# Performance work log

Hardware: AMD Instinct MI355X
Metric: run time of the kernel (lower is better)

The kernel has to match this reference:

```python
import jax, jax.numpy as jnp
import numpy as np

H2 = 512    # internal hidden = hidden_size*2
E = 128     # embedding_size
V = 50000   # vocabulary_size
L = 512     # max_length (encoder input length)
B = 128     # batch


def setup_inputs() -> dict:
    key = jax.random.key(0)
    ks = jax.random.split(key, 20)
    s = 0.02
    return {
        "input_ids": jax.random.randint(ks[0], (B,), 0, V),
        "hidden": jax.random.normal(ks[1], (1, B, H2), jnp.float32),
        "encoder_outputs": jax.random.normal(ks[2], (L, B, H2), jnp.float32),
        "full_input": jax.random.randint(ks[3], (L, B), 0, V),
        # parameters
        "embedding": jax.random.normal(ks[4], (V, E), jnp.float32) * s,
        "W_ih": jax.random.normal(ks[5], (3 * H2, E), jnp.float32) * s,
        "W_hh": jax.random.normal(ks[6], (3 * H2, H2), jnp.float32) * s,
        "b_ih": jnp.zeros((3 * H2,), jnp.float32),
        "b_hh": jnp.zeros((3 * H2,), jnp.float32),
        "W_ds": jax.random.normal(ks[7], (H2, H2), jnp.float32) * s,
        "b_ds": jnp.zeros((H2,), jnp.float32),
        "w_h": jax.random.normal(ks[8], (H2,), jnp.float32),
        "att_v": jax.random.normal(ks[9], (H2,), jnp.float32),
        "W_oh": jax.random.normal(ks[10], (E, 2 * H2), jnp.float32) * s,
        "b_oh": jnp.zeros((E,), jnp.float32),
        "W_ov": jax.random.normal(ks[11], (V, E), jnp.float32) * s,
        "b_ov": jnp.zeros((V,), jnp.float32),
        "W_ptr": jax.random.normal(ks[12], (1, 2 * H2 + E), jnp.float32) * s,
        "b_ptr": jnp.zeros((1,), jnp.float32),
    }


def reference(input_ids, hidden, encoder_outputs, full_input, embedding,
              W_ih, W_hh, b_ih, b_hh, W_ds, b_ds, w_h, att_v,
              W_oh, b_oh, W_ov, b_ov, W_ptr, b_ptr):
    Bn = input_ids.shape[0]
    Ln = encoder_outputs.shape[0]
    Vn = embedding.shape[0]

    emb = embedding[input_ids]                       # [B, E] (dropout = identity in eval)
    h0 = hidden[0]                                   # [B, 2h]

    # single GRU step (PyTorch gate order r, z, n)
    gx = emb @ W_ih.T + b_ih                         # [B, 3*2h]
    gh = h0 @ W_hh.T + b_hh
    xr, xz, xn = jnp.split(gx, 3, axis=1)
    hr, hz, hn = jnp.split(gh, 3, axis=1)
    r = jax.nn.sigmoid(xr + hr)
    z = jax.nn.sigmoid(xz + hz)
    n = jnp.tanh(xn + r * hn)
    h_new = (1.0 - z) * n + z * h0                   # [B, 2h]

    # Bahdanau-style attention (faithful to source, incl. softmax over dim=1 = batch axis)
    dsl = h_new @ W_ds.T + b_ds                      # [B, 2h]
    att = jnp.tanh(w_h * encoder_outputs + dsl[None])  # [L, B, 2h]
    scores = (att_v * att).sum(-1)                   # [L, B]
    attn = jax.nn.softmax(scores, axis=1)            # torch F.softmax(dim=1)

    context = jnp.einsum('lb,lbh->bh', attn, encoder_outputs)  # [B, 2h]
    combined = jnp.concatenate([h_new, context], axis=1)        # [B, 4h]

    p_vocab = jax.nn.softmax((combined @ W_oh.T + b_oh) @ W_ov.T + b_ov, axis=1)  # [B, V]

    p_gen = jax.nn.sigmoid(jnp.concatenate([combined, emb], axis=1) @ W_ptr.T + b_ptr)  # [B, 1]

    # scatter attention mass onto extended vocab (copy distribution)
    token_input_dist = jnp.zeros((Bn, Vn + Ln), p_vocab.dtype).at[
        jnp.arange(Bn)[:, None], full_input.T
    ].add(attn.T)

    pad = jnp.zeros((Bn, Ln), p_vocab.dtype)
    p_final = jnp.concatenate([p_vocab * p_gen, pad], axis=1) + (1.0 - p_gen) * token_input_dist
    return (p_final, h_new[None], attn)
```

## Files before the change

### kernel.cpp

```cpp
#include <hip/hip_runtime.h>
#include <math.h>

#define B_  128
#define E_  128
#define H2_ 512
#define H3_ 1536
#define L_  512
#define V_  50000
#define VL_ 50512

typedef short bf16x8 __attribute__((ext_vector_type(8)));
typedef float f32x4 __attribute__((ext_vector_type(4)));

__device__ __forceinline__ float fast_tanh(float x) {
    float e = __expf(2.f * x);
    return 1.f - 2.f / (e + 1.f);
}
__device__ __forceinline__ float fast_sigmoid(float x) {
    return 1.f / (1.f + __expf(-x));
}
__device__ __forceinline__ short f2bf(float f) {
    unsigned u = __float_as_uint(f);
    u += 0x7fff + ((u >> 16) & 1);
    return (short)(u >> 16);
}

__global__ void k_init(float* __restrict__ gx, float* __restrict__ gh,
                       float* __restrict__ dsl, float* __restrict__ hid,
                       float* __restrict__ out, float* __restrict__ rsum8,
                       const float* __restrict__ b_ih, const float* __restrict__ b_hh,
                       const float* __restrict__ b_ds, const float* __restrict__ b_oh) {
    int i = blockIdx.x * blockDim.x + threadIdx.x;
    if (i < 196608) { gx[i] = b_ih[i % 1536]; return; }
    i -= 196608;
    if (i < 196608) { gh[i] = b_hh[i % 1536]; return; }
    i -= 196608;
    if (i < 65536)  { dsl[i] = b_ds[i & 511]; return; }
    i -= 65536;
    if (i < 16384)  { hid[i] = b_oh[i & 127]; return; }
    i -= 16384;
    if (i < 65536)  { out[(size_t)(i >> 9) * VL_ + V_ + (i & 511)] = 0.f; return; }
    i -= 65536;
    if (i < 1024)   rsum8[i] = 0.f;
}

__global__ void k_gates(const int* __restrict__ ids, const float* __restrict__ tab,
                        const float* __restrict__ hidden,
                        const float* __restrict__ W_ih, const float* __restrict__ W_hh,
                        float* __restrict__ gx, float* __restrict__ gh) {
    __shared__ float As[32][36];
    __shared__ float Ws[32][36];
    int z = blockIdx.z;
    int which = (z < 2) ? 0 : 1;
    int kbeg  = which ? (z - 2) * 128 : z * 64;
    int kiter = which ? 4 : 2;
    const float* W = which ? W_hh : W_ih;
    int ldw = which ? H2_ : E_;
    float* C = which ? gh : gx;
    int bm = blockIdx.x * 32, bn = blockIdx.y * 32;
    int tid = threadIdx.x;
    int tm0 = (tid / 16) * 2, tn0 = (tid % 16) * 2;
    float acc[2][2] = {};
    for (int it = 0; it < kiter; ++it) {
        int k0 = kbeg + it * 32;
        for (int v = tid; v < 256; v += 256) {
            int m = v >> 3, q = (v & 7) << 2;
            int gm = bm + m;
            const float* arow = which ? (hidden + (size_t)gm * H2_)
                                      : (tab + (size_t)ids[gm] * E_);
            float4 x = *(const float4*)(arow + k0 + q);
            As[q+0][m] = x.x; As[q+1][m] = x.y; As[q+2][m] = x.z; As[q+3][m] = x.w;
        }
        for (int v = tid; v < 256; v += 256) {
            int n = v >> 3, q = (v & 7) << 2;
            float4 x = *(const float4*)(W + (size_t)(bn + n) * ldw + k0 + q);
            Ws[q+0][n] = x.x; Ws[q+1][n] = x.y; Ws[q+2][n] = x.z; Ws[q+3][n] = x.w;
        }
        __syncthreads();
        #pragma unroll
        for (int kk = 0; kk < 32; ++kk) {
            float a0 = As[kk][tm0], a1 = As[kk][tm0+1];
            float w0 = Ws[kk][tn0], w1 = Ws[kk][tn0+1];
            acc[0][0] += a0*w0; acc[0][1] += a0*w1;
            acc[1][0] += a1*w0; acc[1][1] += a1*w1;
        }
        __syncthreads();
    }
    #pragma unroll
    for (int i = 0; i < 2; ++i)
        #pragma unroll
        for (int j = 0; j < 2; ++j)
            atomicAdd(&C[(size_t)(bm+tm0+i) * H3_ + bn+tn0+j], acc[i][j]);
}

template<int BM, int BN, int BK, int TM, int TN, int SPLITK>
__global__ void gemm_t(const float* __restrict__ A, int lda,
                       const float* __restrict__ W, int ldw,
                       float* __restrict__ C, int ldc,
                       int N, int K) {
    __shared__ float As[BK][BM + 4];
    __shared__ float Ws[BK][BN + 4];
    int bm = blockIdx.x * BM, bn = blockIdx.y * BN;
    int tid = threadIdx.x;
    constexpr int NT = BN / TN;
    int tm0 = (tid / NT) * TM;
    int tn0 = (tid % NT) * TN;
    int kchunk = K / SPLITK;
    int kbeg = blockIdx.z * kchunk;
    float acc[TM][TN] = {};
    for (int k0 = kbeg; k0 < kbeg + kchunk; k0 += BK) {
        #pragma unroll
        for (int v = tid; v < BM * BK / 4; v += 256) {
            int m = v / (BK / 4), q = (v % (BK / 4)) * 4;
            float4 x = *(const float4*)(A + (size_t)(bm + m) * lda + k0 + q);
            As[q+0][m] = x.x; As[q+1][m] = x.y; As[q+2][m] = x.z; As[q+3][m] = x.w;
        }
        #pragma unroll
        for (int v = tid; v < BN * BK / 4; v += 256) {
            int n = v / (BK / 4), q = (v % (BK / 4)) * 4;
            float4 x = *(const float4*)(W + (size_t)(bn + n) * ldw + k0 + q);
            Ws[q+0][n] = x.x; Ws[q+1][n] = x.y; Ws[q+2][n] = x.z; Ws[q+3][n] = x.w;
        }
        __syncthreads();
        #pragma unroll
        for (int kk = 0; kk < BK; ++kk) {
            float a[TM], w[TN];
            #pragma unroll
            for (int i = 0; i < TM; ++i) a[i] = As[kk][tm0 + i];
            #pragma unroll
            for (int j = 0; j < TN; ++j) w[j] = Ws[kk][tn0 + j];
            #pragma unroll
            for (int i = 0; i < TM; ++i)
                #pragma unroll
                for (int j = 0; j < TN; ++j) acc[i][j] += a[i] * w[j];
        }
        __syncthreads();
    }
    #pragma unroll
    for (int i = 0; i < TM; ++i)
        #pragma unroll
        for (int j = 0; j < TN; ++j)
            atomicAdd(&C[(size_t)(bm+tm0+i) * ldc + bn+tn0+j], acc[i][j]);
}

__global__ void k_gru(const float* __restrict__ gx, const float* __restrict__ gh,
                      const float* __restrict__ h0,
                      float* __restrict__ comb, float* __restrict__ hout) {
    int idx = blockIdx.x * blockDim.x + threadIdx.x;
    int b = idx >> 9, h = idx & 511;
    const float* gxb = gx + b * H3_;
    const float* ghb = gh + b * H3_;
    float xr = gxb[h], xz = gxb[H2_ + h], xn = gxb[2 * H2_ + h];
    float hr = ghb[h], hz = ghb[H2_ + h], hn = ghb[2 * H2_ + h];
    float r = fast_sigmoid(xr + hr);
    float z = fast_sigmoid(xz + hz);
    float n = fast_tanh(xn + r * hn);
    float hv = (1.f - z) * n + z * h0[idx];
    comb[b * (2 * H2_) + h] = hv;
    comb[b * (2 * H2_) + H2_ + h] = 0.f;
    hout[idx] = hv;
}

__global__ void k_scores(const float* __restrict__ enc, const float* __restrict__ dsl,
                         const float* __restrict__ w_h, const float* __restrict__ att_v,
                         float* __restrict__ scores) {
    int wid = (blockIdx.x << 2) + (threadIdx.x >> 6);
    int lane = threadIdx.x & 63;
    int l = wid >> 7, b = wid & 127;
    const float4* e4 = (const float4*)(enc + ((size_t)(l * B_ + b)) * H2_);
    const float4* d4 = (const float4*)(dsl + b * H2_);
    const float4* w4 = (const float4*)w_h;
    const float4* v4 = (const float4*)att_v;
    float s = 0.f;
    #pragma unroll
    for (int i = 0; i < 2; ++i) {
        int j = lane + (i << 6);
        float4 e = e4[j], d = d4[j], w = w4[j], v = v4[j];
        s += v.x * fast_tanh(w.x * e.x + d.x);
        s += v.y * fast_tanh(w.y * e.y + d.y);
        s += v.z * fast_tanh(w.z * e.z + d.z);
        s += v.w * fast_tanh(w.w * e.w + d.w);
    }
    #pragma unroll
    for (int o = 32; o; o >>= 1) s += __shfl_xor(s, o);
    if (lane == 0) scores[l * B_ + b] = s;
}

__global__ void k_softmax(const float* __restrict__ scores, float* __restrict__ attn) {
    int l = blockIdx.x, lane = threadIdx.x;
    float s0 = scores[l * B_ + lane], s1 = scores[l * B_ + lane + 64];
    float m = fmaxf(s0, s1);
    #pragma unroll
    for (int o = 32; o; o >>= 1) m = fmaxf(m, __shfl_xor(m, o));
    float e0 = __expf(s0 - m), e1 = __expf(s1 - m);
    float t = e0 + e1;
    #pragma unroll
    for (int o = 32; o; o >>= 1) t += __shfl_xor(t, o);
    float inv = 1.f / t;
    attn[l * B_ + lane] = e0 * inv;
    attn[l * B_ + lane + 64] = e1 * inv;
}

__global__ void k_context(const float* __restrict__ enc, const float* __restrict__ attn,
                          float* __restrict__ comb) {
    int b = blockIdx.x;
    int l0 = blockIdx.y << 6;
    int tid = threadIdx.x;
    __shared__ float a_s[64];
    if (tid < 64) a_s[tid] = attn[(l0 + tid) * B_ + b];
    __syncthreads();
    const float4* e = (const float4*)(enc + ((size_t)l0 * B_ + b) * H2_) + tid;
    float4 c = make_float4(0.f, 0.f, 0.f, 0.f);
    #pragma unroll 8
    for (int i = 0; i < 64; ++i) {
        float4 x = e[(size_t)i * (B_ * H2_ / 4)];
        float a = a_s[i];
        c.x += a * x.x; c.y += a * x.y; c.z += a * x.z; c.w += a * x.w;
    }
    float* dst = comb + b * (2 * H2_) + H2_ + tid * 4;
    atomicAdd(dst + 0, c.x); atomicAdd(dst + 1, c.y);
    atomicAdd(dst + 2, c.z); atomicAdd(dst + 3, c.w);
}

__global__ void k_pgen(const float* __restrict__ comb,
                       const int* __restrict__ ids, const float* __restrict__ tab,
                       const float* __restrict__ W_ptr, const float* __restrict__ b_ptr,
                       float* __restrict__ pgen) {
    int b = blockIdx.x, lane = threadIdx.x;
    float s = 0.f;
    for (int j = lane; j < 2 * H2_; j += 64) s += W_ptr[j] * comb[b * (2 * H2_) + j];
    const float* erow = tab + (size_t)ids[b] * E_;
    for (int j = lane; j < E_; j += 64) s += W_ptr[2 * H2_ + j] * erow[j];
    #pragma unroll
    for (int o = 32; o; o >>= 1) s += __shfl_xor(s, o);
    if (lane == 0) pgen[b] = fast_sigmoid(s + b_ptr[0]);
}

__global__ void k_vocab(const float* __restrict__ hid, const float* __restrict__ Wov,
                        const float* __restrict__ bov, float* __restrict__ out,
                        float* __restrict__ rsum8) {
    __shared__ float sm[4][128];
    int L = threadIdx.x & 63, w = threadIdx.x >> 6;
    int lrow = L & 15, lk = L >> 4;
    int n0 = blockIdx.x * 128 + w * 32;

    bf16x8 bfr[2][4];
    #pragma unroll
    for (int nt = 0; nt < 2; ++nt) {
        int n = n0 + nt * 16 + lrow;
        #pragma unroll
        for (int kk = 0; kk < 4; ++kk) {
            bf16x8 f;
            if (n < V_) {
                const float* p = Wov + (size_t)n * 128 + kk * 32 + lk * 8;
                float4 x = *(const float4*)p, y = *(const float4*)(p + 4);
                f[0]=f2bf(x.x); f[1]=f2bf(x.y); f[2]=f2bf(x.z); f[3]=f2bf(x.w);
                f[4]=f2bf(y.x); f[5]=f2bf(y.y); f[6]=f2bf(y.z); f[7]=f2bf(y.w);
            } else {
                #pragma unroll
                for (int j = 0; j < 8; ++j) f[j] = 0;
            }
            bfr[nt][kk] = f;
        }
    }
    f32x4 acc[8][2] = {};
    #pragma unroll
    for (int mt = 0; mt < 8; ++mt) {
        bf16x8 afr[4];
        #pragma unroll
        for (int kk = 0; kk < 4; ++kk) {
            const float* p = hid + (size_t)(mt * 16 + lrow) * 128 + kk * 32 + lk * 8;
            float4 x = *(const float4*)p, y = *(const float4*)(p + 4);
            bf16x8 f;
            f[0]=f2bf(x.x); f[1]=f2bf(x.y); f[2]=f2bf(x.z); f[3]=f2bf(x.w);
            f[4]=f2bf(y.x); f[5]=f2bf(y.y); f[6]=f2bf(y.z); f[7]=f2bf(y.w);
            afr[kk] = f;
        }
        #pragma unroll
        for (int nt = 0; nt < 2; ++nt)
            #pragma unroll
            for (int kk = 0; kk < 4; ++kk)
                acc[mt][nt] = __builtin_amdgcn_mfma_f32_16x16x32_bf16(
                    afr[kk], bfr[nt][kk], acc[mt][nt], 0, 0, 0);
    }
    float bv[2];
    #pragma unroll
    for (int nt = 0; nt < 2; ++nt) {
        int n = n0 + nt * 16 + lrow;
        bv[nt] = (n < V_) ? bov[n] : 0.f;
    }
    float rs[8][4];
    #pragma unroll
    for (int mt = 0; mt < 8; ++mt) {
        #pragma unroll
        for (int r = 0; r < 4; ++r) rs[mt][r] = 0.f;
        #pragma unroll
        for (int nt = 0; nt < 2; ++nt) {
            int n = n0 + nt * 16 + lrow;
            if (n < V_) {
                #pragma unroll
                for (int r = 0; r < 4; ++r) {
                    int row = mt * 16 + lk * 4 + r;
                    float e = __expf(acc[mt][nt][r] + bv[nt]);
                    out[(size_t)row * VL_ + n] = e;
                    rs[mt][r] += e;
                }
            }
        }
    }
    #pragma unroll
    for (int o = 1; o < 16; o <<= 1)
        #pragma unroll
        for (int mt = 0; mt < 8; ++mt)
            #pragma unroll
            for (int r = 0; r < 4; ++r) rs[mt][r] += __shfl_xor(rs[mt][r], o);
    if (lrow == 0) {
        #pragma unroll
        for (int mt = 0; mt < 8; ++mt)
            #pragma unroll
            for (int r = 0; r < 4; ++r)
                sm[w][mt * 16 + lk * 4 + r] = rs[mt][r];
    }
    __syncthreads();
    if (threadIdx.x < 128) {
        float p = sm[0][threadIdx.x] + sm[1][threadIdx.x]
                + sm[2][threadIdx.x] + sm[3][threadIdx.x];
        atomicAdd(&rsum8[(blockIdx.x & 7) * 128 + threadIdx.x], p);
    }
}

__global__ void k_final(float* __restrict__ out, const float* __restrict__ pgen,
                        const float* __restrict__ rsum8) {
    int b = blockIdx.y, chunk = blockIdx.x, tid = threadIdx.x;
    __shared__ float sc;
    if (tid == 0) {
        float s = 0.f;
        #pragma unroll
        for (int j = 0; j < 8; ++j) s += rsum8[j * 128 + b];
        sc = pgen[b] / s;
    }
    __syncthreads();
    int j = chunk * 256 + tid;
    if (j < V_ / 4) {
        float4* p = (float4*)(out + (size_t)b * VL_) + j;
        float4 x = *p;
        x.x *= sc; x.y *= sc; x.z *= sc; x.w *= sc;
        *p = x;
    }
}

__global__ void k_scatter(float* __restrict__ out, const int* __restrict__ full_input,
                          const float* __restrict__ attn, const float* __restrict__ pgen) {
    int idx = blockIdx.x * blockDim.x + threadIdx.x;
    int b = idx & 127;
    int tok = full_input[idx];
    atomicAdd(&out[(size_t)b * VL_ + tok], (1.f - pgen[b]) * attn[idx]);
}

extern "C" void kernel_launch(void* const* d_in, const int* in_sizes, int n_in,
                              void* d_out, int out_size, void* d_ws, size_t ws_size,
                              hipStream_t stream) {
    const int*   input_ids = (const int*)d_in[0];
    const float* hidden    = (const float*)d_in[1];
    const float* enc       = (const float*)d_in[2];
    const int*   full_in   = (const int*)d_in[3];
    const float* emb_tab   = (const float*)d_in[4];
    const float* W_ih      = (const float*)d_in[5];
    const float* W_hh      = (const float*)d_in[6];
    const float* b_ih      = (const float*)d_in[7];
    const float* b_hh      = (const float*)d_in[8];
    const float* W_ds      = (const float*)d_in[9];
    const float* b_ds      = (const float*)d_in[10];
    const float* w_h       = (const float*)d_in[11];
    const float* att_v     = (const float*)d_in[12];
    const float* W_oh      = (const float*)d_in[13];
    const float* b_oh      = (const float*)d_in[14];
    const float* W_ov      = (const float*)d_in[15];
    const float* b_ov      = (const float*)d_in[16];
    const float* W_ptr     = (const float*)d_in[17];
    const float* b_ptr     = (const float*)d_in[18];

    float* out = (float*)d_out;
    float* p_final = out;
    float* h_out   = out + (size_t)B_ * VL_;
    float* attn    = out + (size_t)B_ * VL_ + B_ * H2_;

    float* ws = (float*)d_ws;
    float* gx     = ws;
    float* gh     = gx + 196608;
    float* comb   = gh + 196608;
    float* dsl    = comb + 131072;
    float* scores = dsl + 65536;
    float* hid    = scores + 65536;
    float* pgen   = hid + 16384;
    float* rsum8  = pgen + 128;

    k_init<<<dim3(2116), dim3(256), 0, stream>>>(gx, gh, dsl, hid, out, rsum8,
                                                 b_ih, b_hh, b_ds, b_oh);
    k_gates<<<dim3(4,48,6), dim3(256), 0, stream>>>(input_ids, emb_tab, hidden,
                                                    W_ih, W_hh, gx, gh);
    k_gru<<<dim3(256), dim3(256), 0, stream>>>(gx, gh, hidden, comb, h_out);
    gemm_t<32,32,32,2,2,4><<<dim3(4,16,4), dim3(256), 0, stream>>>(
        comb, 2*H2_, W_ds, H2_, dsl, H2_, H2_, H2_);
    k_scores<<<dim3(L_*B_/4), dim3(256), 0, stream>>>(enc, dsl, w_h, att_v, scores);
    k_softmax<<<dim3(L_), dim3(64), 0, stream>>>(scores, attn);
    k_context<<<dim3(B_, 8), dim3(128), 0, stream>>>(enc, attn, comb);
    k_pgen<<<dim3(B_), dim3(64), 0, stream>>>(comb, input_ids, emb_tab, W_ptr, b_ptr, pgen);
    gemm_t<32,32,32,2,2,8><<<dim3(4,4,8), dim3(256), 0, stream>>>(
        comb, 2*H2_, W_oh, 2*H2_, hid, E_, E_, 2*H2_);
    k_vocab<<<dim3(391), dim3(256), 0, stream>>>(hid, W_ov, b_ov, p_final, rsum8);
    k_final<<<dim3(49, 128), dim3(256), 0, stream>>>(p_final, pgen, rsum8);
    k_scatter<<<dim3(L_*B_/256), dim3(256), 0, stream>>>(p_final, full_in, attn, pgen);
}
```

Measured before the change: 144.5 us.

## Stage vocab exponentials in fp16 scratch, batch 8 rows per score wave, split context finer

k_vocab now writes the unnormalised exponentials to an fp16 scratch buffer instead of the fp32 output, and k_final reads that buffer and writes the scaled fp32 result. Before, the fp32 output was written, read back and rewritten; now the intermediate round trip moves half the bytes. k_scores has each wave handle 8 encoder rows, so the dsl, w_h and att_v loads are amortised and more loads are in flight. k_context splits L into 32 chunks of 16 for more parallelism, at the cost of more atomics, and the fp16 staging of values in [0, e^max] risks overflow or lost precision.

```diff
diff --git a/kernel.cpp b/kernel.cpp
--- a/kernel.cpp
+++ b/kernel.cpp
@@ -1,4 +1,5 @@
 #include <hip/hip_runtime.h>
+#include <hip/hip_fp16.h>
 #include <math.h>
 
 #define B_  128
@@ -11,6 +12,7 @@
 
 typedef short bf16x8 __attribute__((ext_vector_type(8)));
 typedef float f32x4 __attribute__((ext_vector_type(4)));
+typedef _Float16 half4 __attribute__((ext_vector_type(4)));
 
 __device__ __forceinline__ float fast_tanh(float x) {
     float e = __expf(2.f * x);
@@ -166,24 +168,42 @@
                          float* __restrict__ scores) {
     int wid = (blockIdx.x << 2) + (threadIdx.x >> 6);
     int lane = threadIdx.x & 63;
-    int l = wid >> 7, b = wid & 127;
-    const float4* e4 = (const float4*)(enc + ((size_t)(l * B_ + b)) * H2_);
+    int b = wid & 127, lg = wid >> 7;
+    int l0 = lg << 3;
     const float4* d4 = (const float4*)(dsl + b * H2_);
     const float4* w4 = (const float4*)w_h;
     const float4* v4 = (const float4*)att_v;
-    float s = 0.f;
-    #pragma unroll
-    for (int i = 0; i < 2; ++i) {
-        int j = lane + (i << 6);
-        float4 e = e4[j], d = d4[j], w = w4[j], v = v4[j];
-        s += v.x * fast_tanh(w.x * e.x + d.x);
-        s += v.y * fast_tanh(w.y * e.y + d.y);
-        s += v.z * fast_tanh(w.z * e.z + d.z);
-        s += v.w * fast_tanh(w.w * e.w + d.w);
-    }
-    #pragma unroll
-    for (int o = 32; o; o >>= 1) s += __shfl_xor(s, o);
-    if (lane == 0) scores[l * B_ + b] = s;
+    float4 d0 = d4[lane], d1 = d4[lane + 64];
+    float4 w0 = w4[lane], w1 = w4[lane + 64];
+    float4 v0 = v4[lane], v1 = v4[lane + 64];
+    float4 e0[8], e1[8];
+    #pragma unroll
+    for (int q = 0; q < 8; ++q) {
+        const float4* e4 = (const float4*)(enc + ((size_t)((l0 + q) * B_ + b)) * H2_);
+        e0[q] = e4[lane];
+        e1[q] = e4[lane + 64];
+    }
+    float s[8];
+    #pragma unroll
+    for (int q = 0; q < 8; ++q) {
+        float t;
+        t  = v0.x * fast_tanh(w0.x * e0[q].x + d0.x);
+        t += v0.y * fast_tanh(w0.y * e0[q].y + d0.y);
+        t += v0.z * fast_tanh(w0.z * e0[q].z + d0.z);
+        t += v0.w * fast_tanh(w0.w * e0[q].w + d0.w);
+        t += v1.x * fast_tanh(w1.x * e1[q].x + d1.x);
+        t += v1.y * fast_tanh(w1.y * e1[q].y + d1.y);
+        t += v1.z * fast_tanh(w1.z * e1[q].z + d1.z);
+        t += v1.w * fast_tanh(w1.w * e1[q].w + d1.w);
+        s[q] = t;
+    }
+    #pragma unroll
+    for (int q = 0; q < 8; ++q) {
+        float t = s[q];
+        #pragma unroll
+        for (int o = 32; o; o >>= 1) t += __shfl_xor(t, o);
+        if (lane == 0) scores[(l0 + q) * B_ + b] = t;
+    }
 }
 
 __global__ void k_softmax(const float* __restrict__ scores, float* __restrict__ attn) {
@@ -204,15 +224,15 @@
 __global__ void k_context(const float* __restrict__ enc, const float* __restrict__ attn,
                           float* __restrict__ comb) {
     int b = blockIdx.x;
-    int l0 = blockIdx.y << 6;
+    int l0 = blockIdx.y << 4;
     int tid = threadIdx.x;
-    __shared__ float a_s[64];
-    if (tid < 64) a_s[tid] = attn[(l0 + tid) * B_ + b];
+    __shared__ float a_s[16];
+    if (tid < 16) a_s[tid] = attn[(l0 + tid) * B_ + b];
     __syncthreads();
     const float4* e = (const float4*)(enc + ((size_t)l0 * B_ + b) * H2_) + tid;
     float4 c = make_float4(0.f, 0.f, 0.f, 0.f);
-    #pragma unroll 8
-    for (int i = 0; i < 64; ++i) {
+    #pragma unroll
+    for (int i = 0; i < 16; ++i) {
         float4 x = e[(size_t)i * (B_ * H2_ / 4)];
         float a = a_s[i];
         c.x += a * x.x; c.y += a * x.y; c.z += a * x.z; c.w += a * x.w;
@@ -237,7 +257,7 @@
 }
 
 __global__ void k_vocab(const float* __restrict__ hid, const float* __restrict__ Wov,
-                        const float* __restrict__ bov, float* __restrict__ out,
+                        const float* __restrict__ bov, _Float16* __restrict__ eout,
                         float* __restrict__ rsum8) {
     __shared__ float sm[4][128];
     int L = threadIdx.x & 63, w = threadIdx.x >> 6;
@@ -302,7 +322,7 @@
                 for (int r = 0; r < 4; ++r) {
                     int row = mt * 16 + lk * 4 + r;
                     float e = __expf(acc[mt][nt][r] + bv[nt]);
-                    out[(size_t)row * VL_ + n] = e;
+                    eout[(size_t)row * V_ + n] = (_Float16)e;
                     rs[mt][r] += e;
                 }
             }
@@ -329,8 +349,8 @@
     }
 }
 
-__global__ void k_final(float* __restrict__ out, const float* __restrict__ pgen,
-                        const float* __restrict__ rsum8) {
+__global__ void k_final(const _Float16* __restrict__ eout, float* __restrict__ out,
+                        const float* __restrict__ pgen, const float* __restrict__ rsum8) {
     int b = blockIdx.y, chunk = blockIdx.x, tid = threadIdx.x;
     __shared__ float sc;
     if (tid == 0) {
@@ -342,10 +362,11 @@
     __syncthreads();
     int j = chunk * 256 + tid;
     if (j < V_ / 4) {
-        float4* p = (float4*)(out + (size_t)b * VL_) + j;
-        float4 x = *p;
-        x.x *= sc; x.y *= sc; x.z *= sc; x.w *= sc;
-        *p = x;
+        half4 h = ((const half4*)(eout + (size_t)b * V_))[j];
+        float4 x;
+        x.x = (float)h[0] * sc; x.y = (float)h[1] * sc;
+        x.z = (float)h[2] * sc; x.w = (float)h[3] * sc;
+        ((float4*)(out + (size_t)b * VL_))[j] = x;
     }
 }
 
@@ -394,6 +415,7 @@
     float* hid    = scores + 65536;
     float* pgen   = hid + 16384;
     float* rsum8  = pgen + 128;
+    _Float16* eout = (_Float16*)(rsum8 + 1024);
 
     k_init<<<dim3(2116), dim3(256), 0, stream>>>(gx, gh, dsl, hid, out, rsum8,
                                                  b_ih, b_hh, b_ds, b_oh);
@@ -402,13 +424,13 @@
     k_gru<<<dim3(256), dim3(256), 0, stream>>>(gx, gh, hidden, comb, h_out);
     gemm_t<32,32,32,2,2,4><<<dim3(4,16,4), dim3(256), 0, stream>>>(
         comb, 2*H2_, W_ds, H2_, dsl, H2_, H2_, H2_);
-    k_scores<<<dim3(L_*B_/4), dim3(256), 0, stream>>>(enc, dsl, w_h, att_v, scores);
+    k_scores<<<dim3(2048), dim3(256), 0, stream>>>(enc, dsl, w_h, att_v, scores);
     k_softmax<<<dim3(L_), dim3(64), 0, stream>>>(scores, attn);
-    k_context<<<dim3(B_, 8), dim3(128), 0, stream>>>(enc, attn, comb);
+    k_context<<<dim3(B_, 32), dim3(128), 0, stream>>>(enc, attn, comb);
     k_pgen<<<dim3(B_), dim3(64), 0, stream>>>(comb, input_ids, emb_tab, W_ptr, b_ptr, pgen);
     gemm_t<32,32,32,2,2,8><<<dim3(4,4,8), dim3(256), 0, stream>>>(
         comb, 2*H2_, W_oh, 2*H2_, hid, E_, E_, 2*H2_);
-    k_vocab<<<dim3(391), dim3(256), 0, stream>>>(hid, W_ov, b_ov, p_final, rsum8);
-    k_final<<<dim3(49, 128), dim3(256), 0, stream>>>(p_final, pgen, rsum8);
+    k_vocab<<<dim3(391), dim3(256), 0, stream>>>(hid, W_ov, b_ov, eout, rsum8);
+    k_final<<<dim3(49, 128), dim3(256), 0, stream>>>(eout, p_final, pgen, rsum8);
     k_scatter<<<dim3(L_*B_/256), dim3(256), 0, stream>>>(p_final, full_in, attn, pgen);
 }
```

Result: slower. 155.3 us (+7.4%).
